# Performance work log

Measured on AMD Instinct MI355X. Metric: run time of the kernel, lower is better.

## Reference

```python
import jax, jax.numpy as jnp
from jax import lax
import numpy as np

V, H, L = 32000, 512, 256   # vocab, hidden_dim, latent_dim
B, TE, TD = 16, 512, 256    # batch, enc max len, dec max len


def setup_inputs() -> dict:
    key = jax.random.key(0)
    ks = jax.random.split(key, 20)
    s = 0.05
    inp = {}
    inp['emb'] = jax.random.normal(ks[0], (V, H), jnp.float32) * s
    # GRU params, PyTorch layout: W_ih [3H_out, D_in], gate order r,z,n
    inp['enc_Wih'] = jax.random.normal(ks[1], (3 * H, H), jnp.float32) * s
    inp['enc_Whh'] = jax.random.normal(ks[2], (3 * H, H), jnp.float32) * s
    inp['enc_bih'] = jnp.zeros((3 * H,), jnp.float32)
    inp['enc_bhh'] = jnp.zeros((3 * H,), jnp.float32)
    inp['dec_Wih'] = jax.random.normal(ks[3], (3 * L, H), jnp.float32) * s
    inp['dec_Whh'] = jax.random.normal(ks[4], (3 * L, L), jnp.float32) * s
    inp['dec_bih'] = jnp.zeros((3 * L,), jnp.float32)
    inp['dec_bhh'] = jnp.zeros((3 * L,), jnp.float32)
    inp['W_mu'] = jax.random.normal(ks[5], (L, 2 * H), jnp.float32) * s
    inp['b_mu'] = jnp.zeros((L,), jnp.float32)
    inp['W_ls'] = jax.random.normal(ks[6], (L, 2 * H), jnp.float32) * s
    inp['b_ls'] = jnp.zeros((L,), jnp.float32)
    inp['W_fc'] = jax.random.normal(ks[7], (V, L), jnp.float32) * s
    inp['b_fc'] = jnp.zeros((V,), jnp.float32)
    inp['noise'] = jax.random.normal(ks[8], (B, L), jnp.float32)  # reparam eps
    inp['enc_ids'] = jax.random.randint(ks[9], (B, TE), 0, V)
    inp['enc_len'] = jax.random.randint(ks[10], (B,), 1, TE + 1)
    inp['dec_ids'] = jax.random.randint(ks[11], (B, TD), 0, V)
    inp['dec_len'] = jax.random.randint(ks[12], (B,), 1, TD + 1)
    return inp


def gru(x, lengths, h0, Wih, Whh, bih, bhh):
    # x: [B,T,D], h0: [B,Hout]. Emulates packed GRU: state frozen and output
    # zeroed past each sample's length (pad_packed_sequence semantics).
    T = x.shape[1]
    Hout = h0.shape[-1]
    xT = jnp.swapaxes(x, 0, 1)                              # [T,B,D]
    valid = jnp.arange(T)[:, None] < lengths[None, :]       # [T,B]

    def step(h, inp):
        x_t, v = inp
        gx = x_t @ Wih.T + bih                              # [B,3Hout]
        gh = h @ Whh.T + bhh
        r = jax.nn.sigmoid(gx[:, :Hout] + gh[:, :Hout])
        z = jax.nn.sigmoid(gx[:, Hout:2 * Hout] + gh[:, Hout:2 * Hout])
        n = jnp.tanh(gx[:, 2 * Hout:] + r * gh[:, 2 * Hout:])
        h_new = (1.0 - z) * n + z * h
        h_keep = jnp.where(v[:, None], h_new, h)
        out = jnp.where(v[:, None], h_new, 0.0)
        return h_keep, out

    h_last, outs = lax.scan(step, h0, (xT, valid))
    return jnp.swapaxes(outs, 0, 1), h_last                 # [B,T,Hout], [B,Hout]


def masked_softmax(scores, mask):
    s = jnp.where(mask, scores, -jnp.inf)
    a = jax.nn.softmax(s, axis=-1)
    return jnp.where(mask, a, 0.0)


def reference(emb, enc_Wih, enc_Whh, enc_bih, enc_bhh,
              dec_Wih, dec_Whh, dec_bih, dec_bhh,
              W_mu, b_mu, W_ls, b_ls, W_fc, b_fc, noise,
              enc_ids, enc_len, dec_ids, dec_len):
    # ---- encode ----
    x_enc = emb[enc_ids]                                    # [B,TE,H]
    h0 = jnp.zeros((x_enc.shape[0], H), x_enc.dtype)
    out, last_state = gru(x_enc, enc_len, h0, enc_Wih, enc_Whh, enc_bih, enc_bhh)
    mask = jnp.arange(out.shape[1])[None, :] < enc_len[:, None]   # [B,TE]
    # batched masked attention pooling (replaces per-sample _return_weight loop)
    first_state = out[:, 0, :]                              # out[0] always valid
    alpha_fw = masked_softmax(jnp.einsum('btd,bd->bt', out, last_state), mask)
    alpha_bw = masked_softmax(jnp.einsum('btd,bd->bt', out, first_state), mask)
    alpha = 0.5 * (alpha_fw + alpha_bw)
    semantic = jnp.einsum('bt,btd->bd', alpha, out)
    h_enc = jnp.concatenate([last_state, semantic], axis=1)  # [B,2H]
    # ---- sample latent ----
    mu = h_enc @ W_mu.T + b_mu
    sigma = jnp.exp(h_enc @ W_ls.T + b_ls)
    z = mu + sigma * noise
    # ---- decode ----
    x_dec = emb[dec_ids]                                    # [B,TD,H]
    dec_out, _ = gru(x_dec, dec_len, z, dec_Wih, dec_Whh, dec_bih, dec_bhh)
    logits = dec_out @ W_fc.T + b_fc                        # [B,TD,V]
    dec_max_len = jnp.max(dec_len)
    return logits, dec_max_len, mu, sigma
```

## Files before the change

### kernel.cpp

```cpp
#include <hip/hip_runtime.h>
#include <hip/hip_bf16.h>
#include <stdint.h>

#define B 16
#define H 512
#define L 256
#define TE 512
#define TD 256
#define NV 32000

typedef __attribute__((ext_vector_type(8))) __bf16 bf16x8;
typedef __attribute__((ext_vector_type(4))) float f32x4;
typedef __attribute__((ext_vector_type(8))) unsigned short u16x8;
typedef __attribute__((ext_vector_type(4))) unsigned short u16x4;
typedef unsigned short u16;
typedef unsigned long long u64;

__device__ __forceinline__ u16 f2bf(float f) {
  unsigned u = __float_as_uint(f);
  u += 0x7fffu + ((u >> 16) & 1u);
  return (u16)(u >> 16);
}
__device__ __forceinline__ float fast_sigmoid(float x) {
  return __builtin_amdgcn_rcpf(1.f + __expf(-x));
}
__device__ __forceinline__ float fast_tanh(float x) {
  float e = __expf(2.f * x);
  return 1.f - 2.f * __builtin_amdgcn_rcpf(e + 1.f);
}

__device__ __forceinline__ u16x8 pack8(float4 a, float4 c) {
  u16x8 r;
  r[0] = f2bf(a.x); r[1] = f2bf(a.y); r[2] = f2bf(a.z); r[3] = f2bf(a.w);
  r[4] = f2bf(c.x); r[5] = f2bf(c.y); r[6] = f2bf(c.z); r[7] = f2bf(c.w);
  return r;
}

__global__ __launch_bounds__(256) void k_f2bf(const float* __restrict__ in,
                                              u16* __restrict__ outp, long n) {
  long i = ((long)blockIdx.x * 256 + threadIdx.x) * 8;
  if (i + 8 > n) return;
  float4 a = *(const float4*)&in[i];
  float4 c = *(const float4*)&in[i + 4];
  *(u16x8*)&outp[i] = pack8(a, c);
}

__global__ __launch_bounds__(256) void k_gather(const float* __restrict__ emb,
                                                const int* __restrict__ ids,
                                                u16* __restrict__ X, int rows) {
  int gid = blockIdx.x * 256 + threadIdx.x;
  int m = gid >> 6, seg = gid & 63;
  if (m >= rows) return;
  long src = (long)ids[m] * H + seg * 8;
  float4 a = *(const float4*)&emb[src];
  float4 c = *(const float4*)&emb[src + 4];
  *(u16x8*)&X[(long)m * H + seg * 8] = pack8(a, c);
}

__device__ __forceinline__ void gemm_tile(char* smem, int bx, int by,
                                          const u16* __restrict__ A,
                                          const u16* __restrict__ Bw,
                                          const float* __restrict__ bias,
                                          float* __restrict__ C,
                                          int N, int K) {
  constexpr int LDSK = 72;
  u16* Al = (u16*)smem;
  u16* Bl = (u16*)(smem + 128 * LDSK * 2);
  const int tid = threadIdx.x;
  const int lane = tid & 63;
  const int wave = tid >> 6;
  const int wr = (wave >> 1) * 64, wc = (wave & 1) * 64;
  const long tM = (long)by * 128, tN = (long)bx * 128;
  const int r32 = tid >> 3;
  const int c8 = (tid & 7) * 8;
  const u16* Ag = A + (tM + r32) * (long)K + c8;
  const u16* Bg = Bw + (tN + r32) * (long)K + c8;
  const int fr = lane & 15;
  const int fq = lane >> 4;
  f32x4 acc[4][4] = {};

  for (int kb = 0; kb < K; kb += 64) {
    u16x8 ta0 = *(const u16x8*)(Ag + kb);
    u16x8 ta1 = *(const u16x8*)(Ag + 32 * (long)K + kb);
    u16x8 ta2 = *(const u16x8*)(Ag + 64 * (long)K + kb);
    u16x8 ta3 = *(const u16x8*)(Ag + 96 * (long)K + kb);
    u16x8 tb0 = *(const u16x8*)(Bg + kb);
    u16x8 tb1 = *(const u16x8*)(Bg + 32 * (long)K + kb);
    u16x8 tb2 = *(const u16x8*)(Bg + 64 * (long)K + kb);
    u16x8 tb3 = *(const u16x8*)(Bg + 96 * (long)K + kb);
    __syncthreads();
    *(u16x8*)&Al[(r32 +  0) * LDSK + c8] = ta0;
    *(u16x8*)&Al[(r32 + 32) * LDSK + c8] = ta1;
    *(u16x8*)&Al[(r32 + 64) * LDSK + c8] = ta2;
    *(u16x8*)&Al[(r32 + 96) * LDSK + c8] = ta3;
    *(u16x8*)&Bl[(r32 +  0) * LDSK + c8] = tb0;
    *(u16x8*)&Bl[(r32 + 32) * LDSK + c8] = tb1;
    *(u16x8*)&Bl[(r32 + 64) * LDSK + c8] = tb2;
    *(u16x8*)&Bl[(r32 + 96) * LDSK + c8] = tb3;
    __syncthreads();
#pragma unroll
    for (int ks = 0; ks < 2; ks++) {
      const int kcol = ks * 32 + fq * 8;
      bf16x8 av[4], bv[4];
#pragma unroll
      for (int mi = 0; mi < 4; mi++)
        av[mi] = __builtin_bit_cast(bf16x8, *(const u16x8*)&Al[(wr + mi * 16 + fr) * LDSK + kcol]);
#pragma unroll
      for (int ni = 0; ni < 4; ni++)
        bv[ni] = __builtin_bit_cast(bf16x8, *(const u16x8*)&Bl[(wc + ni * 16 + fr) * LDSK + kcol]);
#pragma unroll
      for (int mi = 0; mi < 4; mi++)
#pragma unroll
        for (int ni = 0; ni < 4; ni++)
          acc[mi][ni] = __builtin_amdgcn_mfma_f32_16x16x32_bf16(av[mi], bv[ni], acc[mi][ni], 0, 0, 0);
    }
  }
#pragma unroll
  for (int mi = 0; mi < 4; mi++) {
    long row = tM + wr + mi * 16 + fq * 4;
#pragma unroll
    for (int ni = 0; ni < 4; ni++) {
      long col = tN + wc + ni * 16 + fr;
      float bs = bias[col];
#pragma unroll
      for (int r = 0; r < 4; r++)
        C[(row + r) * (long)N + col] = acc[mi][ni][r] + bs;
    }
  }
}

__global__ __launch_bounds__(256) void k_gemm_bt(const u16* __restrict__ A,
                                                 const u16* __restrict__ Bw,
                                                 const float* __restrict__ bias,
                                                 float* __restrict__ C,
                                                 int M, int N, int K) {
  __shared__ __align__(16) char smem[2 * 128 * 72 * 2];
  gemm_tile(smem, blockIdx.x, blockIdx.y, A, Bw, bias, C, N, K);
}

template <bool ENC, int HD, int T, int UPW>
__global__ __launch_bounds__(256) void k_gru10(const float* __restrict__ GX,
                                               const float* __restrict__ Whh,
                                               const float* __restrict__ bhh,
                                               const int* __restrict__ lens,
                                               u64* __restrict__ Hbuf,
                                               const float* __restrict__ h0f,
                                               float* __restrict__ out_f32,
                                               u16* __restrict__ out_bf,
                                               float* __restrict__ hlast,
                                               int ngru,
                                               const u16* __restrict__ sA,
                                               const u16* __restrict__ sB,
                                               const float* __restrict__ sbias,
                                               float* __restrict__ sC,
                                               const float* __restrict__ cvt_in,
                                               u16* __restrict__ cvt_out) {
  constexpr int ROWS = 3 * UPW;
  constexpr int NT = ROWS / 16;
  constexpr int NA = (NT + 3) / 4;
  constexpr int LDH = HD + 8;
  constexpr int CT = 16 * UPW / 2;
  constexpr int WPB = HD / 2;
  constexpr int NWORD = 16 * WPB;
  constexpr int PW = NWORD / 256;
  constexpr size_t WB = (size_t)ROWS * LDH * 2;
  constexpr size_t HBB = (size_t)16 * LDH * 2;
  constexpr size_t GB = (size_t)3 * 16 * UPW * 4;
  constexpr size_t GRUB = WB + HBB + GB;
  constexpr size_t SMEMB = GRUB > 36864 ? GRUB : 36864;
  __shared__ __align__(16) char smem[SMEMB];

  if ((int)blockIdx.x >= ngru) {
    int sb = (int)blockIdx.x - ngru;
    if (sb < 192) {
      gemm_tile(smem, sb % 6, sb / 6, sA, sB, sbias, sC, 3 * L, H);
    } else {
      int sbf = sb - 192;
      for (long base = (long)sbf * 2048 + (long)threadIdx.x * 8;
           base < (long)NV * L; base += 240L * 2048) {
        float4 a = *(const float4*)&cvt_in[base];
        float4 c = *(const float4*)&cvt_in[base + 4];
        *(u16x8*)&cvt_out[base] = pack8(a, c);
      }
    }
    return;
  }

  u16 (*w_lds)[LDH] = (u16(*)[LDH])smem;
  u16 (*h_lds)[LDH] = (u16(*)[LDH])(smem + WB);
  float (*g_lds)[16][UPW] = (float(*)[16][UPW])(smem + WB + HBB);

  const int tid = threadIdx.x;
  const int u0 = blockIdx.x * UPW;
  const int lane = tid & 63, wv = tid >> 6;
  const int fr = lane & 15, fq = lane >> 4;

  for (int i = tid; i < ROWS * HD / 4; i += 256) {
    int rr = i / (HD / 4), c = (i % (HD / 4)) * 4;
    int grow = (rr / UPW) * HD + u0 + (rr % UPW);
    float4 v = *(const float4*)&Whh[(long)grow * HD + c];
    u16x4 p; p[0] = f2bf(v.x); p[1] = f2bf(v.y); p[2] = f2bf(v.z); p[3] = f2bf(v.w);
    *(u16x4*)&w_lds[rr][c] = p;
  }
  int tmax = 1;
#pragma unroll
  for (int i = 0; i < 16; i++) tmax = max(tmax, lens[i]);

  const bool act = tid < CT;
  const int cb = tid / (UPW / 2);
  const int up = tid % (UPW / 2);
  const int uu = u0 + 2 * up;
  const int len_b = lens[act ? cb : 0];
  float bh[3][2], hold[2];
#pragma unroll
  for (int g = 0; g < 3; g++)
#pragma unroll
    for (int j = 0; j < 2; j++) bh[g][j] = act ? bhh[g * HD + uu + j] : 0.f;
#pragma unroll
  for (int j = 0; j < 2; j++)
    hold[j] = (ENC || !act) ? 0.f : h0f[cb * HD + uu + j];
  __syncthreads();

  for (int t = 0; ; t++) {
    const u64* Hc = Hbuf + (size_t)(t & 1) * NWORD;
    u64* Hn = Hbuf + (size_t)((t + 1) & 1) * NWORD;
    float gxv[3][2];
    if (act) {
#pragma unroll
      for (int g = 0; g < 3; g++)
#pragma unroll
        for (int j = 0; j < 2; j++)
          gxv[g][j] = GX[((size_t)cb * T + t) * 3 * HD + g * HD + uu + j];
    }
    const unsigned want = (unsigned)t;
    u64 vv[PW];
#pragma unroll
    for (int i = 0; i < PW; i++)
      vv[i] = __hip_atomic_load(&Hc[i * 256 + tid], __ATOMIC_RELAXED, __HIP_MEMORY_SCOPE_AGENT);
    for (;;) {
      bool ok = true;
#pragma unroll
      for (int i = 0; i < PW; i++) ok &= ((unsigned)(vv[i] >> 32) == want);
      if (ok) break;
#pragma unroll
      for (int i = 0; i < PW; i++)
        if ((unsigned)(vv[i] >> 32) != want)
          vv[i] = __hip_atomic_load(&Hc[i * 256 + tid], __ATOMIC_RELAXED, __HIP_MEMORY_SCOPE_AGENT);
    }
#pragma unroll
    for (int i = 0; i < PW; i++) {
      int w = i * 256 + tid;
      *(unsigned*)&h_lds[w / WPB][(w % WPB) * 2] = (unsigned)vv[i];
    }
    __syncthreads();
    f32x4 acc[NA];
#pragma unroll
    for (int a = 0; a < NA; a++) {
      int ti = wv + a * 4;
      if (ti < NT) {
        f32x4 ac = {};
#pragma unroll
        for (int kk = 0; kk < HD / 32; kk++) {
          int kc = kk * 32 + fq * 8;
          bf16x8 av = __builtin_bit_cast(bf16x8, *(const u16x8*)&h_lds[fr][kc]);
          bf16x8 bv = __builtin_bit_cast(bf16x8, *(const u16x8*)&w_lds[ti * 16 + fr][kc]);
          ac = __builtin_amdgcn_mfma_f32_16x16x32_bf16(av, bv, ac, 0, 0, 0);
        }
        acc[a] = ac;
      }
    }
#pragma unroll
    for (int a = 0; a < NA; a++) {
      int ti = wv + a * 4;
      if (ti < NT) {
        int g = (ti * 16) / UPW, ul = (ti * 16) % UPW;
#pragma unroll
        for (int r = 0; r < 4; r++)
          g_lds[g][fq * 4 + r][ul + fr] = acc[a][r];
      }
    }
    __syncthreads();
    if (act) {
      const bool val = t < len_b;
      u16 pk[2]; float hnv[2];
#pragma unroll
      for (int j = 0; j < 2; j++) {
        int u = 2 * up + j;
        float rr_ = fast_sigmoid(g_lds[0][cb][u] + bh[0][j] + gxv[0][j]);
        float zz  = fast_sigmoid(g_lds[1][cb][u] + bh[1][j] + gxv[1][j]);
        float nn  = fast_tanh(gxv[2][j] + rr_ * (g_lds[2][cb][u] + bh[2][j]));
        float hnew = (1.f - zz) * nn + zz * hold[j];
        float hk = val ? hnew : hold[j];
        hold[j] = hk;
        pk[j] = f2bf(hk);
        hnv[j] = val ? hnew : 0.f;
      }
      u64 pw = ((u64)(unsigned)(t + 1) << 32) | ((unsigned)pk[1] << 16) | pk[0];
      __hip_atomic_store(&Hn[cb * WPB + (uu >> 1)], pw,
                         __ATOMIC_RELAXED, __HIP_MEMORY_SCOPE_AGENT);
      if constexpr (ENC) {
        *(float2*)&out_f32[((size_t)cb * T + t) * HD + uu] = make_float2(hnv[0], hnv[1]);
      } else {
        *(unsigned*)&out_bf[((size_t)cb * T + t) * HD + uu] =
            ((unsigned)f2bf(hnv[1]) << 16) | f2bf(hnv[0]);
      }
    }
    if (t + 1 >= tmax) break;
  }

  if (act) {
    if constexpr (ENC) {
      *(float2*)&hlast[cb * HD + uu] = make_float2(hold[0], hold[1]);
      for (int t2 = tmax; t2 < T; t2++)
        *(float2*)&out_f32[((size_t)cb * T + t2) * HD + uu] = make_float2(0.f, 0.f);
    } else {
      for (int t2 = tmax; t2 < T; t2++)
        *(unsigned*)&out_bf[((size_t)cb * T + t2) * HD + uu] = 0u;
    }
  }
}

__global__ __launch_bounds__(256) void k_middle(const float* __restrict__ out_enc,
                                                const float* __restrict__ hlast,
                                                const int* __restrict__ enc_len,
                                                const float* __restrict__ W_mu,
                                                const float* __restrict__ b_mu,
                                                const float* __restrict__ W_ls,
                                                const float* __restrict__ b_ls,
                                                const float* __restrict__ noise,
                                                const int* __restrict__ dec_len,
                                                float* __restrict__ out_tail,
                                                float* __restrict__ zf,
                                                u64* __restrict__ hbw) {
  const int b = blockIdx.x, tid = threadIdx.x;
  __shared__ float last[H], first[H], sfw[TE], sbw[TE], alpha[TE], sem[H];
  __shared__ float redA[256], redB[256];
  __shared__ u16 zbf[L];
  const int len = enc_len[b];
  for (int i = tid; i < H; i += 256) {
    last[i] = hlast[b * H + i];
    first[i] = out_enc[((size_t)b * TE) * H + i];
  }
  __syncthreads();
  for (int t = tid; t < TE; t += 256) {
    float afw = 0.f, abw = 0.f;
    if (t < len) {
      const float4* op = (const float4*)&out_enc[((size_t)b * TE + t) * H];
      for (int i = 0; i < H / 4; i++) {
        float4 o = op[i];
        float4 l = *(const float4*)&last[i * 4];
        float4 f = *(const float4*)&first[i * 4];
        afw += o.x * l.x + o.y * l.y + o.z * l.z + o.w * l.w;
        abw += o.x * f.x + o.y * f.y + o.z * f.z + o.w * f.w;
      }
    }
    sfw[t] = afw; sbw[t] = abw;
  }
  __syncthreads();
  float mfw = -3e38f, mbw = -3e38f;
  for (int t = tid; t < len; t += 256) { mfw = fmaxf(mfw, sfw[t]); mbw = fmaxf(mbw, sbw[t]); }
  redA[tid] = mfw; redB[tid] = mbw; __syncthreads();
  for (int s = 128; s > 0; s >>= 1) {
    if (tid < s) { redA[tid] = fmaxf(redA[tid], redA[tid + s]); redB[tid] = fmaxf(redB[tid], redB[tid + s]); }
    __syncthreads();
  }
  const float Mfw = redA[0], Mbw = redB[0];
  __syncthreads();
  float tfw = 0.f, tbw = 0.f;
  for (int t = tid; t < len; t += 256) {
    float e1 = expf(sfw[t] - Mfw); sfw[t] = e1; tfw += e1;
    float e2 = expf(sbw[t] - Mbw); sbw[t] = e2; tbw += e2;
  }
  redA[tid] = tfw; redB[tid] = tbw; __syncthreads();
  for (int s = 128; s > 0; s >>= 1) {
    if (tid < s) { redA[tid] += redA[tid + s]; redB[tid] += redB[tid + s]; }
    __syncthreads();
  }
  const float ifw = 0.5f / redA[0], ibw = 0.5f / redB[0];
  __syncthreads();
  for (int t = tid; t < TE; t += 256) alpha[t] = (t < len) ? (sfw[t] * ifw + sbw[t] * ibw) : 0.f;
  __syncthreads();
  for (int d = tid; d < H; d += 256) {
    float s = 0.f;
    for (int t = 0; t < len; t++) s += alpha[t] * out_enc[((size_t)b * TE + t) * H + d];
    sem[d] = s;
  }
  __syncthreads();
  {
    const int j = tid;
    const float4* wm = (const float4*)&W_mu[(size_t)j * 2 * H];
    const float4* wl = (const float4*)&W_ls[(size_t)j * 2 * H];
    float am = 0.f, al = 0.f;
    for (int i = 0; i < H / 4; i++) {
      float4 hh = *(const float4*)&last[i * 4];
      float4 w1 = wm[i]; am += hh.x * w1.x + hh.y * w1.y + hh.z * w1.z + hh.w * w1.w;
      float4 w2 = wl[i]; al += hh.x * w2.x + hh.y * w2.y + hh.z * w2.z + hh.w * w2.w;
    }
    for (int i = 0; i < H / 4; i++) {
      float4 hh = *(const float4*)&sem[i * 4];
      float4 w1 = wm[H / 4 + i]; am += hh.x * w1.x + hh.y * w1.y + hh.z * w1.z + hh.w * w1.w;
      float4 w2 = wl[H / 4 + i]; al += hh.x * w2.x + hh.y * w2.y + hh.z * w2.z + hh.w * w2.w;
    }
    float muv = am + b_mu[j];
    float sgv = expf(al + b_ls[j]);
    float zv = muv + sgv * noise[b * L + j];
    out_tail[131072001ul + (size_t)b * L + j] = muv;
    out_tail[131076097ul + (size_t)b * L + j] = sgv;
    zf[b * L + j] = zv;
    zbf[j] = f2bf(zv);
  }
  __syncthreads();
  if (tid < L / 2) {
    u64 pw = ((unsigned)zbf[2 * tid + 1] << 16) | (u64)zbf[2 * tid];
    __hip_atomic_store(&hbw[b * (L / 2) + tid], pw,
                       __ATOMIC_RELAXED, __HIP_MEMORY_SCOPE_AGENT);
  }
  if (b == 0 && tid == 0) {
    int m = 0;
    for (int i = 0; i < B; i++) m = max(m, dec_len[i]);
    out_tail[131072000ul] = (float)m;
  }
}

extern "C" void kernel_launch(void* const* d_in, const int* in_sizes, int n_in,
                              void* d_out, int out_size, void* d_ws, size_t ws_size,
                              hipStream_t stream) {
  const float* emb     = (const float*)d_in[0];
  const float* eWih    = (const float*)d_in[1];
  const float* eWhh    = (const float*)d_in[2];
  const float* ebih    = (const float*)d_in[3];
  const float* ebhh    = (const float*)d_in[4];
  const float* dWih    = (const float*)d_in[5];
  const float* dWhh    = (const float*)d_in[6];
  const float* dbih    = (const float*)d_in[7];
  const float* dbhh    = (const float*)d_in[8];
  const float* W_mu    = (const float*)d_in[9];
  const float* b_mu    = (const float*)d_in[10];
  const float* W_ls    = (const float*)d_in[11];
  const float* b_ls    = (const float*)d_in[12];
  const float* W_fc    = (const float*)d_in[13];
  const float* b_fc    = (const float*)d_in[14];
  const float* noise   = (const float*)d_in[15];
  const int*   enc_ids = (const int*)d_in[16];
  const int*   enc_len = (const int*)d_in[17];
  const int*   dec_ids = (const int*)d_in[18];
  const int*   dec_len = (const int*)d_in[19];
  float* out = (float*)d_out;
  char* ws = (char*)d_ws;

  u16*   eWih_bf  = (u16*)(ws + 0);
  u16*   dWih_bf  = (u16*)(ws + 1572864);
  u16*   Wfc_bf   = (u16*)(ws + 2359296);
  u64*   Hbuf_enc = (u64*)(ws + 18743296);
  float* hlast    = (float*)(ws + 18808832);
  u64*   Hbuf_dec = (u64*)(ws + 18841600);
  u16*   dec_out  = (u16*)(ws + 18874368);
  float* zf       = (float*)(ws + 20971520);

  char* ob = (char*)d_out;
  u16*   Xenc_bf = (u16*)(ob + 0);
  u16*   Xdec_bf = (u16*)(ob + 8388608);
  float* GXE     = (float*)(ob + 12582912);
  float* GXD     = (float*)(ob + 62914560);
  float* out_enc = (float*)(ob + 75497472);

  hipMemsetAsync(Hbuf_enc, 0, 65536, stream);
  hipMemsetAsync(Hbuf_dec, 0, 32768, stream);

  k_f2bf<<<384, 256, 0, stream>>>(eWih, eWih_bf, 786432);
  k_f2bf<<<192, 256, 0, stream>>>(dWih, dWih_bf, 393216);
  k_gather<<<2048, 256, 0, stream>>>(emb, enc_ids, Xenc_bf, B * TE);
  k_gather<<<1024, 256, 0, stream>>>(emb, dec_ids, Xdec_bf, B * TD);

  k_gemm_bt<<<dim3(12, 64), 256, 0, stream>>>(Xenc_bf, eWih_bf, ebih, GXE, B * TE, 3 * H, H);

  k_gru10<true, H, TE, 32><<<448, 256, 0, stream>>>(GXE, eWhh, ebhh, enc_len, Hbuf_enc,
                                                    nullptr, out_enc, nullptr, hlast,
                                                    16, Xdec_bf, dWih_bf, dbih, GXD,
                                                    W_fc, Wfc_bf);

  k_middle<<<B, 256, 0, stream>>>(out_enc, hlast, enc_len, W_mu, b_mu, W_ls, b_ls,
                                  noise, dec_len, out, zf, Hbuf_dec);

  k_gru10<false, L, TD, 16><<<16, 256, 0, stream>>>(GXD, dWhh, dbhh, dec_len, Hbuf_dec,
                                                    zf, nullptr, dec_out, nullptr,
                                                    16, nullptr, nullptr, nullptr, nullptr,
                                                    nullptr, nullptr);

  k_gemm_bt<<<dim3(250, 32), 256, 0, stream>>>(dec_out, Wfc_bf, b_fc, out, B * TD, NV, L);
}
```

Before: 2.171 ms.

## Overlap decoder GRU with vocab projection GEMM via progress flags

The decoder GRU kernel now launches extra side blocks that compute the final logits GEMM. The GEMM is split into two halves of time steps, and each half is gated on per-block progress counters that the GRU blocks publish at step 128 and at the end. This removes the separate logits GEMM launch and hides part of it behind the serial recurrence. Padding-zero writes are redistributed across all threads. The cost is spin-wait polling, atomic stores, and reliance on co-residency of the GRU and side blocks.

Measured after the change: 2.209 ms. About the same (+1.7%).

```diff
diff --git a/kernel.cpp b/kernel.cpp
--- a/kernel.cpp
+++ b/kernel.cpp
@@ -139,7 +139,7 @@
 }
 
 template <bool ENC, int HD, int T, int UPW>
-__global__ __launch_bounds__(256) void k_gru10(const float* __restrict__ GX,
+__global__ __launch_bounds__(256) void k_gru11(const float* __restrict__ GX,
                                                const float* __restrict__ Whh,
                                                const float* __restrict__ bhh,
                                                const int* __restrict__ lens,
@@ -154,7 +154,8 @@
                                                const float* __restrict__ sbias,
                                                float* __restrict__ sC,
                                                const float* __restrict__ cvt_in,
-                                               u16* __restrict__ cvt_out) {
+                                               u16* __restrict__ cvt_out,
+                                               unsigned* __restrict__ prog) {
   constexpr int ROWS = 3 * UPW;
   constexpr int NT = ROWS / 16;
   constexpr int NA = (NT + 3) / 4;
@@ -170,17 +171,43 @@
   constexpr size_t SMEMB = GRUB > 36864 ? GRUB : 36864;
   __shared__ __align__(16) char smem[SMEMB];
 
+  const int tid = threadIdx.x;
+
   if ((int)blockIdx.x >= ngru) {
-    int sb = (int)blockIdx.x - ngru;
-    if (sb < 192) {
-      gemm_tile(smem, sb % 6, sb / 6, sA, sB, sbias, sC, 3 * L, H);
+    if constexpr (ENC) {
+      int sb = (int)blockIdx.x - ngru;
+      if (sb < 192) {
+        gemm_tile(smem, sb % 6, sb / 6, sA, sB, sbias, sC, 3 * L, H);
+      } else {
+        int sbf = sb - 192;
+        for (long base = (long)sbf * 2048 + (long)tid * 8;
+             base < (long)NV * L; base += 240L * 2048) {
+          float4 a = *(const float4*)&cvt_in[base];
+          float4 c = *(const float4*)&cvt_in[base + 4];
+          *(u16x8*)&cvt_out[base] = pack8(a, c);
+        }
+      }
     } else {
-      int sbf = sb - 192;
-      for (long base = (long)sbf * 2048 + (long)threadIdx.x * 8;
-           base < (long)NV * L; base += 240L * 2048) {
-        float4 a = *(const float4*)&cvt_in[base];
-        float4 c = *(const float4*)&cvt_in[base + 4];
-        *(u16x8*)&cvt_out[base] = pack8(a, c);
+      const int sid = (int)blockIdx.x - ngru;
+      const int nside = (int)gridDim.x - ngru;
+      auto gate = [&](unsigned need) {
+        for (;;) {
+          unsigned p = 2u;
+          if (tid < 16)
+            p = __hip_atomic_load(&prog[tid * 16], __ATOMIC_RELAXED, __HIP_MEMORY_SCOPE_AGENT);
+          if (__syncthreads_and((int)(p >= need))) break;
+          __builtin_amdgcn_s_sleep(16);
+        }
+      };
+      for (int e = sid; e < 4000; e += nside) {
+        int by = 2 * (e / 250), bx = e % 250;
+        gate(1u);
+        gemm_tile(smem, bx, by, sA, sB, sbias, sC, NV, L);
+      }
+      for (int o = sid; o < 4000; o += nside) {
+        int by = 2 * (o / 250) + 1, bx = o % 250;
+        gate(2u);
+        gemm_tile(smem, bx, by, sA, sB, sbias, sC, NV, L);
       }
     }
     return;
@@ -190,7 +217,6 @@
   u16 (*h_lds)[LDH] = (u16(*)[LDH])(smem + WB);
   float (*g_lds)[16][UPW] = (float(*)[16][UPW])(smem + WB + HBB);
 
-  const int tid = threadIdx.x;
   const int u0 = blockIdx.x * UPW;
   const int lane = tid & 63, wv = tid >> 6;
   const int fr = lane & 15, fq = lane >> 4;
@@ -301,8 +327,19 @@
       if constexpr (ENC) {
         *(float2*)&out_f32[((size_t)cb * T + t) * HD + uu] = make_float2(hnv[0], hnv[1]);
       } else {
-        *(unsigned*)&out_bf[((size_t)cb * T + t) * HD + uu] =
-            ((unsigned)f2bf(hnv[1]) << 16) | f2bf(hnv[0]);
+        unsigned ow = ((unsigned)f2bf(hnv[1]) << 16) | f2bf(hnv[0]);
+        __hip_atomic_store((unsigned*)&out_bf[((size_t)cb * T + t) * HD + uu], ow,
+                           __ATOMIC_RELAXED, __HIP_MEMORY_SCOPE_AGENT);
+      }
+    }
+    if constexpr (!ENC) {
+      if (t + 1 == 128) {
+        asm volatile("s_waitcnt vmcnt(0)" ::: "memory");
+        __builtin_amdgcn_sched_barrier(0);
+        __syncthreads();
+        if (tid == 0)
+          __hip_atomic_store(&prog[blockIdx.x * 16], 1u,
+                             __ATOMIC_RELAXED, __HIP_MEMORY_SCOPE_AGENT);
       }
     }
     if (t + 1 >= tmax) break;
@@ -311,12 +348,28 @@
   if (act) {
     if constexpr (ENC) {
       *(float2*)&hlast[cb * HD + uu] = make_float2(hold[0], hold[1]);
-      for (int t2 = tmax; t2 < T; t2++)
-        *(float2*)&out_f32[((size_t)cb * T + t2) * HD + uu] = make_float2(0.f, 0.f);
-    } else {
-      for (int t2 = tmax; t2 < T; t2++)
-        *(unsigned*)&out_bf[((size_t)cb * T + t2) * HD + uu] = 0u;
-    }
+    }
+  }
+  if constexpr (ENC) {
+    float4 z4 = make_float4(0.f, 0.f, 0.f, 0.f);
+    for (int bb = 0; bb < 16; bb++)
+      for (int x = tid; x < (T - tmax) * HD / 4; x += 256) {
+        int t2 = tmax + (x * 4) / HD, c = (x * 4) % HD;
+        *(float4*)&out_f32[((size_t)bb * T + t2) * HD + c] = z4;
+      }
+  } else {
+    for (int bb = 0; bb < 16; bb++)
+      for (int x = tid; x < (T - tmax) * HD / 4; x += 256) {
+        int t2 = tmax + (x * 4) / HD, c = (x * 4) % HD;
+        __hip_atomic_store((u64*)&out_bf[((size_t)bb * T + t2) * HD + c], 0ull,
+                           __ATOMIC_RELAXED, __HIP_MEMORY_SCOPE_AGENT);
+      }
+    asm volatile("s_waitcnt vmcnt(0)" ::: "memory");
+    __builtin_amdgcn_sched_barrier(0);
+    __syncthreads();
+    if (tid == 0)
+      __hip_atomic_store(&prog[blockIdx.x * 16], 2u,
+                         __ATOMIC_RELAXED, __HIP_MEMORY_SCOPE_AGENT);
   }
 }
 
@@ -456,16 +509,18 @@
   u64*   Hbuf_dec = (u64*)(ws + 18841600);
   u16*   dec_out  = (u16*)(ws + 18874368);
   float* zf       = (float*)(ws + 20971520);
+  unsigned* prog  = (unsigned*)(ws + 20987904);
 
   char* ob = (char*)d_out;
   u16*   Xenc_bf = (u16*)(ob + 0);
   u16*   Xdec_bf = (u16*)(ob + 8388608);
   float* GXE     = (float*)(ob + 12582912);
-  float* GXD     = (float*)(ob + 62914560);
   float* out_enc = (float*)(ob + 75497472);
+  float* GXD     = (float*)(ob + 511705088);
 
   hipMemsetAsync(Hbuf_enc, 0, 65536, stream);
   hipMemsetAsync(Hbuf_dec, 0, 32768, stream);
+  hipMemsetAsync(prog, 0, 1024, stream);
 
   k_f2bf<<<384, 256, 0, stream>>>(eWih, eWih_bf, 786432);
   k_f2bf<<<192, 256, 0, stream>>>(dWih, dWih_bf, 393216);
@@ -474,18 +529,16 @@
 
   k_gemm_bt<<<dim3(12, 64), 256, 0, stream>>>(Xenc_bf, eWih_bf, ebih, GXE, B * TE, 3 * H, H);
 
-  k_gru10<true, H, TE, 32><<<448, 256, 0, stream>>>(GXE, eWhh, ebhh, enc_len, Hbuf_enc,
+  k_gru11<true, H, TE, 32><<<448, 256, 0, stream>>>(GXE, eWhh, ebhh, enc_len, Hbuf_enc,
                                                     nullptr, out_enc, nullptr, hlast,
                                                     16, Xdec_bf, dWih_bf, dbih, GXD,
-                                                    W_fc, Wfc_bf);
+                                                    W_fc, Wfc_bf, nullptr);
 
   k_middle<<<B, 256, 0, stream>>>(out_enc, hlast, enc_len, W_mu, b_mu, W_ls, b_ls,
                                   noise, dec_len, out, zf, Hbuf_dec);
 
-  k_gru10<false, L, TD, 16><<<16, 256, 0, stream>>>(GXD, dWhh, dbhh, dec_len, Hbuf_dec,
-                                                    zf, nullptr, dec_out, nullptr,
-                                                    16, nullptr, nullptr, nullptr, nullptr,
-                                                    nullptr, nullptr);
-
-  k_gemm_bt<<<dim3(250, 32), 256, 0, stream>>>(dec_out, Wfc_bf, b_fc, out, B * TD, NV, L);
-}
+  k_gru11<false, L, TD, 16><<<744, 256, 0, stream>>>(GXD, dWhh, dbhh, dec_len, Hbuf_dec,
+                                                     zf, nullptr, dec_out, nullptr,
+                                                     16, dec_out, Wfc_bf, b_fc, out,
+                                                     nullptr, nullptr, prog);
+}
```
